# Optimization experiments

Hardware: AMD Instinct MI355X
Metric: run time of the kernel (lower is better)

## Reference

```python
import jax, jax.numpy as jnp
import numpy as np

B, N, D = 8, 4096, 512      # batch, bag_size, model dim (in_dim == att_dim)
H, DH = 8, 64               # heads, dim_head
M = 256                     # landmarks (N % M == 0 -> no padding branch)
PINV_ITERS = 6
CONV_K = 33                 # residual depthwise conv kernel (lucidrains default)


def layernorm(x, g, b, eps=1e-5):
    mu = x.mean(-1, keepdims=True)
    var = ((x - mu) ** 2).mean(-1, keepdims=True)
    return (x - mu) * jax.lax.rsqrt(var + eps) * g + b


def moore_penrose_pinv(x, iters):
    # iterative Newton-Schulz pseudo-inverse, global max normalization as in lucidrains
    abs_x = jnp.abs(x)
    col = abs_x.sum(-1)
    row = abs_x.sum(-2)
    z = jnp.swapaxes(x, -1, -2) / (jnp.max(col) * jnp.max(row))
    I = jnp.eye(x.shape[-1], dtype=x.dtype)
    for _ in range(iters):
        xz = x @ z
        z = 0.25 * z @ (13.0 * I - xz @ (15.0 * I - xz @ (7.0 * I - xz)))
    return z


def setup_inputs() -> dict:
    key = jax.random.key(0)
    ks = jax.random.split(key, 12)
    s = 0.02
    return {
        "X": jax.random.normal(ks[0], (B, N, D), dtype=jnp.float32),
        "Wqkv": jax.random.normal(ks[1], (D, 3 * H * DH), dtype=jnp.float32) * s,
        "Wout": jax.random.normal(ks[2], (H * DH, D), dtype=jnp.float32) * s,
        "bout": jnp.zeros((D,), dtype=jnp.float32),
        "conv_w": jax.random.normal(ks[3], (H, 1, CONV_K, 1), dtype=jnp.float32) * s,
        "g1": jnp.ones((D,), dtype=jnp.float32),
        "beta1": jnp.zeros((D,), dtype=jnp.float32),
        "g2": jnp.ones((D,), dtype=jnp.float32),
        "beta2": jnp.zeros((D,), dtype=jnp.float32),
        "W1": jax.random.normal(ks[4], (D, 4 * D), dtype=jnp.float32) * s,
        "b1": jnp.zeros((4 * D,), dtype=jnp.float32),
        "W2": jax.random.normal(ks[5], (4 * D, D), dtype=jnp.float32) * s,
        "b2": jnp.zeros((D,), dtype=jnp.float32),
    }


def nystrom_attention(x, Wqkv, Wout, bout, conv_w):
    b, n, _ = x.shape
    qkv = x @ Wqkv                                   # (b, n, 3*H*DH)
    qkv = qkv.reshape(b, n, 3, H, DH)
    q = jnp.transpose(qkv[:, :, 0], (0, 2, 1, 3))    # (b, H, n, DH)
    k = jnp.transpose(qkv[:, :, 1], (0, 2, 1, 3))
    v = jnp.transpose(qkv[:, :, 2], (0, 2, 1, 3))
    q = q * (DH ** -0.5)

    l = n // M  # group size per landmark
    q_l = q.reshape(b, H, M, l, DH).mean(axis=3)     # (b, H, M, DH)
    k_l = k.reshape(b, H, M, l, DH).mean(axis=3)

    sim1 = jnp.einsum("bhnd,bhmd->bhnm", q, k_l)     # (b, H, n, M)
    sim2 = jnp.einsum("bhmd,bhld->bhml", q_l, k_l)   # (b, H, M, M)
    sim3 = jnp.einsum("bhmd,bhnd->bhmn", q_l, k)     # (b, H, M, n)

    attn1 = jax.nn.softmax(sim1, axis=-1)
    attn2 = jax.nn.softmax(sim2, axis=-1)
    attn3 = jax.nn.softmax(sim3, axis=-1)

    attn2_inv = moore_penrose_pinv(attn2, PINV_ITERS)
    out = (attn1 @ attn2_inv) @ (attn3 @ v)          # (b, H, n, DH)

    # residual depthwise conv over sequence dim, heads as channels
    res = jax.lax.conv_general_dilated(
        v, conv_w, window_strides=(1, 1),
        padding=((CONV_K // 2, CONV_K // 2), (0, 0)),
        dimension_numbers=("NCHW", "OIHW", "NCHW"),
        feature_group_count=H,
    )
    out = out + res

    out = jnp.transpose(out, (0, 2, 1, 3)).reshape(b, n, H * DH)
    return out @ Wout + bout


def reference(X, Wqkv, Wout, bout, conv_w, g1, beta1, g2, beta2, W1, b1, W2, b2):
    h = layernorm(X, g1, beta1)
    h = nystrom_attention(h, Wqkv, Wout, bout, conv_w)
    # MLP with residual (use_mlp=True); dropout=0.0 -> identity
    m = layernorm(h, g2, beta2)
    m = jax.nn.gelu(m @ W1 + b1, approximate=False) @ W2 + b2
    h = h + m
    # proj_out is Identity since out_dim == att_dim
    return h
```

## Files before the change

### kernel.cpp

```cpp
#include <hip/hip_runtime.h>
#include <hip/hip_bf16.h>
#include <cmath>

#define DEV __device__ __forceinline__

namespace {

constexpr int kB = 8, kN = 4096, kD = 512, kH = 8, kDH = 64, kM = 256, kL = 16, kCK = 33;
constexpr int kBN = kB * kN;
constexpr int kBH = kB * kH;
constexpr int kHD = kH * kDH;
constexpr int kD4 = 4 * kD;
constexpr int kQKVC = 3 * kHD;

typedef __attribute__((ext_vector_type(8))) short short8;
typedef __attribute__((ext_vector_type(4))) float f32x4;

DEV float toF(float x) { return x; }
DEV float toF(__hip_bfloat16 x) { return __bfloat162float(x); }
DEV __hip_bfloat16 f2b(float f) { return __float2bfloat16(f); }
DEV short f2s(float f) {
  __hip_bfloat16 h = __float2bfloat16(f);
  return *reinterpret_cast<short*>(&h);
}
DEV float us2f(unsigned short u) { return __uint_as_float((unsigned)u << 16); }
DEV unsigned short f2us(float f) {
  __hip_bfloat16 h = __float2bfloat16(f);
  return *reinterpret_cast<unsigned short*>(&h);
}

DEV void gload16(const void* g, void* l) {
  __builtin_amdgcn_global_load_lds(
      (const __attribute__((address_space(1))) unsigned*)g,
      (__attribute__((address_space(3))) unsigned*)l, 16, 0, 0);
}

DEV float waveSum(float v) {
#pragma unroll
  for (int o = 32; o > 0; o >>= 1) v += __shfl_down(v, o, 64);
  return v;
}
DEV float waveMax(float v) {
#pragma unroll
  for (int o = 32; o > 0; o >>= 1) v = fmaxf(v, __shfl_down(v, o, 64));
  return v;
}
DEV float blockSum(float v, float* sb) {
  v = waveSum(v);
  int lane = threadIdx.x & 63, w = threadIdx.x >> 6;
  __syncthreads();
  if (lane == 0) sb[w] = v;
  __syncthreads();
  return sb[0] + sb[1] + sb[2] + sb[3];
}
DEV float blockMax(float v, float* sb) {
  v = waveMax(v);
  int lane = threadIdx.x & 63, w = threadIdx.x >> 6;
  __syncthreads();
  if (lane == 0) sb[w] = v;
  __syncthreads();
  return fmaxf(fmaxf(sb[0], sb[1]), fmaxf(sb[2], sb[3]));
}

__global__ __launch_bounds__(256) void detect_k(const unsigned* __restrict__ x,
                                                int* __restrict__ flag) {
  __shared__ int sc[4];
  int t = threadIdx.x;
  int cb = 0;
  for (int i = t; i < 4096; i += 256) {
    unsigned w = x[i];
    float b0 = __uint_as_float(w << 16);
    float b1 = __uint_as_float(w & 0xffff0000u);
    if (fabsf(b0) < 64.0f && (b0 == 0.0f || fabsf(b0) > 1e-20f)) cb++;
    if (fabsf(b1) < 64.0f && (b1 == 0.0f || fabsf(b1) > 1e-20f)) cb++;
  }
#pragma unroll
  for (int o = 32; o > 0; o >>= 1) cb += __shfl_down(cb, o, 64);
  if ((t & 63) == 0) sc[t >> 6] = cb;
  __syncthreads();
  if (t == 0) flag[0] = (sc[0] + sc[1] + sc[2] + sc[3] > 7373) ? 1 : 0;
}

__global__ void cvt_any_k(const void* __restrict__ s, float* __restrict__ d, int n,
                          const int* __restrict__ flag) {
  int i = blockIdx.x * 256 + threadIdx.x;
  if (i >= n) return;
  if (*flag)
    d[i] = toF(((const __hip_bfloat16*)s)[i]);
  else
    d[i] = ((const float*)s)[i];
}

__global__ void cvtT_k(const void* __restrict__ s, __hip_bfloat16* __restrict__ d, int K, int N,
                       const int* __restrict__ flag) {
  int i = blockIdx.x * 256 + threadIdx.x;
  if (i >= N * K) return;
  int n = i / K, k = i - n * K;
  float v = (*flag) ? toF(((const __hip_bfloat16*)s)[(long)k * N + n])
                    : ((const float*)s)[(long)k * N + n];
  d[i] = f2b(v);
}

__global__ void f32tob16_k(const float* __restrict__ s, __hip_bfloat16* __restrict__ d, int n) {
  int i = blockIdx.x * 256 + threadIdx.x;
  if (i < n) d[i] = f2b(s[i]);
}


__global__ __launch_bounds__(256) void ln1_k(const void* __restrict__ xv,
                                             const float* __restrict__ g,
                                             const float* __restrict__ be,
                                             __hip_bfloat16* __restrict__ o,
                                             const int* __restrict__ flag) {
  __shared__ float sb[4];
  size_t row = blockIdx.x;
  __hip_bfloat16* po = o + row * kD;
  int t = threadIdx.x;
  float v0, v1;
  if (*flag) {
    const __hip_bfloat16* pr = (const __hip_bfloat16*)xv + row * kD;
    v0 = toF(pr[t]);
    v1 = toF(pr[t + 256]);
  } else {
    const float* pr = (const float*)xv + row * kD;
    v0 = pr[t];
    v1 = pr[t + 256];
  }
  float s = blockSum(v0 + v1, sb);
  float ss = blockSum(v0 * v0 + v1 * v1, sb);
  float mu = s * (1.0f / kD);
  float var = ss * (1.0f / kD) - mu * mu;
  float rs = rsqrtf(var + 1e-5f);
  po[t] = f2b((v0 - mu) * rs * g[t] + be[t]);
  po[t + 256] = f2b((v1 - mu) * rs * g[t + 256] + be[t + 256]);
}

__global__ __launch_bounds__(256) void ln2_k(const float* __restrict__ x,
                                             const float* __restrict__ g,
                                             const float* __restrict__ be,
                                             __hip_bfloat16* __restrict__ o) {
  __shared__ float sb[4];
  size_t row = blockIdx.x;
  const float* pr = x + row * kD;
  __hip_bfloat16* po = o + row * kD;
  int t = threadIdx.x;
  float v0 = pr[t], v1 = pr[t + 256];
  float s = blockSum(v0 + v1, sb);
  float ss = blockSum(v0 * v0 + v1 * v1, sb);
  float mu = s * (1.0f / kD);
  float var = ss * (1.0f / kD) - mu * mu;
  float rs = rsqrtf(var + 1e-5f);
  po[t] = f2b((v0 - mu) * rs * g[t] + be[t]);
  po[t + 256] = f2b((v1 - mu) * rs * g[t + 256] + be[t + 256]);
}


__global__ void landmark_k(const __hip_bfloat16* __restrict__ src, float* __restrict__ dst) {
  int i = blockIdx.x * 256 + threadIdx.x;
  if (i >= kBH * kM * kDH) return;
  int dh = i & 63, m = (i >> 6) & 255, bh = i >> 14;
  const __hip_bfloat16* p = src + ((size_t)bh * kN + m * kL) * kDH + dh;
  float s = 0.f;
#pragma unroll
  for (int l = 0; l < kL; ++l) s += toF(p[l * kDH]);
  dst[i] = s * (1.0f / kL);
}

__global__ __launch_bounds__(256) void softmax_k(float* __restrict__ X, int ncols) {
  __shared__ float sb[4];
  size_t row = blockIdx.x;
  float* p = X + row * ncols;
  int t = threadIdx.x;
  float mx = -1e30f;
  for (int c = t; c < ncols; c += 256) mx = fmaxf(mx, p[c]);
  mx = blockMax(mx, sb);
  float s = 0.f;
  for (int c = t; c < ncols; c += 256) {
    float e = expf(fminf(p[c] - mx, 0.0f));
    p[c] = e;
    s += e;
  }
  s = blockSum(s, sb);
  float inv = 1.0f / s;
  for (int c = t; c < ncols; c += 256) p[c] *= inv;
}

__global__ __launch_bounds__(256) void pinv_rowcol_k(const float* __restrict__ a2,
                                                     float* __restrict__ rsum,
                                                     float* __restrict__ csum) {
  __shared__ float sb[4];
  int bh = blockIdx.x >> 8, i = blockIdx.x & 255;
  const float* base = a2 + ((size_t)bh << 16);
  int t = threadIdx.x;
  float rs = blockSum(fabsf(base[i * kM + t]), sb);
  float cs = blockSum(fabsf(base[t * kM + i]), sb);
  if (t == 0) {
    rsum[blockIdx.x] = rs;
    csum[blockIdx.x] = cs;
  }
}

__global__ __launch_bounds__(256) void pinv_gmax_k(const float* __restrict__ rsum,
                                                   const float* __restrict__ csum,
                                                   float* __restrict__ gmax) {
  __shared__ float sb[4];
  int t = threadIdx.x;
  float a = 0.f, b = 0.f;
  for (int j = t; j < kBH * kM; j += 256) {
    a = fmaxf(a, rsum[j]);
    b = fmaxf(b, csum[j]);
  }
  a = blockMax(a, sb);
  b = blockMax(b, sb);
  if (t == 0) {
    gmax[0] = a;
    gmax[1] = b;
  }
}

__global__ void pinv_init_k(const float* __restrict__ a2, const float* __restrict__ gmax,
                            __hip_bfloat16* __restrict__ z) {
  int i = blockIdx.x * 256 + threadIdx.x;
  if (i >= kBH * kM * kM) return;
  int col = i & 255, r = (i >> 8) & 255, bh = i >> 16;
  float denom = fmaxf(gmax[0] * gmax[1], 1e-30f);
  z[i] = f2b(a2[((size_t)bh << 16) + col * kM + r] / denom);
}

constexpr int kCR = 128;
constexpr int kCHA = kCK / 2;
constexpr int kCW = kCR + 2 * kCHA;
constexpr int kCP = 72;

__global__ __launch_bounds__(256) void conv_add2_k(const __hip_bfloat16* __restrict__ v,
                                                   const float* __restrict__ w,
                                                   __hip_bfloat16* __restrict__ ao) {
  __shared__ short Vt[kCW * kCP];
  __shared__ float wsh[kCK];
  const int t = threadIdx.x;
  const int bh = blockIdx.x >> 5;
  const int n0 = (blockIdx.x & 31) * kCR;
  const int b = bh >> 3, h = bh & 7;
  if (t < kCK) wsh[t] = w[h * kCK + t];
  const __hip_bfloat16* vbase = v + (size_t)bh * kN * kDH;
#pragma unroll
  for (int u = 0; u < (kCW * 8 + 255) / 256; ++u) {
    const int idx = u * 256 + t;
    if (idx < kCW * 8) {
      const int r = idx >> 3, c8 = (idx & 7) * 8;
      const int n = n0 - kCHA + r;
      uint4 d = {0u, 0u, 0u, 0u};
      if (n >= 0 && n < kN) d = *(const uint4*)(vbase + (size_t)n * kDH + c8);
      *(uint4*)&Vt[r * kCP + c8] = d;
    }
  }
  __syncthreads();
  const int dh8 = (t & 7) * 8;
  const int rg = (t >> 3) * 4;
  float acc[4][8] = {};
#pragma unroll
  for (int wd = 0; wd < kCK + 3; ++wd) {
    short8 v8 = *(const short8*)&Vt[(rg + wd) * kCP + dh8];
    float f[8];
#pragma unroll
    for (int e = 0; e < 8; ++e) f[e] = us2f((unsigned short)v8[e]);
#pragma unroll
    for (int i = 0; i < 4; ++i) {
      const int tap = wd - i;
      if (tap >= 0 && tap < kCK) {
        const float wt = wsh[tap];
#pragma unroll
        for (int e = 0; e < 8; ++e) acc[i][e] = fmaf(f[e], wt, acc[i][e]);
      }
    }
  }
#pragma unroll
  for (int i = 0; i < 4; ++i) {
    const int n = n0 + rg + i;
    __hip_bfloat16* ap = ao + ((size_t)(b * kN + n)) * kHD + h * kDH + dh8;
    uint4 d = *(const uint4*)ap;
    const unsigned short* us = (const unsigned short*)&d;
    unsigned short ov[8];
#pragma unroll
    for (int e = 0; e < 8; ++e) ov[e] = f2us(us2f(us[e]) + acc[i][e]);
    *(uint4*)ap = *(const uint4*)ov;
  }
}

constexpr int FP = 72;

template <bool A3>
__global__ __launch_bounds__(256, 1) void fattn_k(const __hip_bfloat16* __restrict__ Qp,
                                                  const __hip_bfloat16* __restrict__ Kp,
                                                  const __hip_bfloat16* __restrict__ Vp,
                                                  void* __restrict__ Op) {
  __shared__ __align__(16) char smem[111616];
  short* Ks = (short*)smem;
  short* Vs = (short*)(smem + 36864);
  short* Ps = (short*)(smem + 73728);
  float* wred = (float*)(smem + 110592);
  float* Comb = (float*)smem;

  const int t = threadIdx.x;
  const int lane = t & 63, wave = t >> 6;
  const int l15 = lane & 15, quad = lane >> 4;
  const int bh = A3 ? (blockIdx.x >> 2) : (blockIdx.x >> 6);
  const int q0 = A3 ? ((blockIdx.x & 3) * 64) : ((blockIdx.x & 63) * 64);
  const int NTILES = A3 ? (kN / 256) : 1;
  short* Psw = Ps + wave * 64 * FP;

  short8 aq[4][2];
#pragma unroll
  for (int i = 0; i < 4; ++i) {
    const long qrow = (A3 ? ((long)bh * kM) : ((long)bh * kN)) + q0 + i * 16 + l15;
#pragma unroll
    for (int s = 0; s < 2; ++s)
      aq[i][s] = *(const short8*)(Qp + qrow * kDH + quad * 8 + s * 32);
  }

  f32x4 o[4][4] = {};
  float mrow[4][4], lrow[4][4];
#pragma unroll
  for (int i = 0; i < 4; ++i)
#pragma unroll
    for (int rg = 0; rg < 4; ++rg) {
      mrow[i][rg] = -1e30f;
      lrow[i][rg] = 0.f;
    }

  const long kvbase = (long)bh * (A3 ? kN : kM) * kDH;

  for (int tile = 0; tile < NTILES; ++tile) {
    {
      const int r = t >> 2, c = (t & 3) * 16;
#pragma unroll
      for (int p = 0; p < 4; ++p) {
        const int rr = p * 64 + r;
        const long src = kvbase + (long)(tile * 256 + rr) * kDH + c;
        const uint4* ks = (const uint4*)(Kp + src);
        const uint4* vs = (const uint4*)(Vp + src);
        *(uint4*)&Ks[rr * FP + c] = ks[0];
        *(uint4*)&Ks[rr * FP + c + 8] = ks[1];
        *(uint4*)&Vs[rr * FP + c] = vs[0];
        *(uint4*)&Vs[rr * FP + c + 8] = vs[1];
      }
    }
    __syncthreads();

    f32x4 sacc[4][4] = {};
#pragma unroll
    for (int s = 0; s < 2; ++s) {
      short8 bk[4];
#pragma unroll
      for (int j = 0; j < 4; ++j)
        bk[j] = *(const short8*)&Ks[(wave * 64 + j * 16 + l15) * FP + quad * 8 + s * 32];
#pragma unroll
      for (int i = 0; i < 4; ++i)
#pragma unroll
        for (int j = 0; j < 4; ++j)
          sacc[i][j] =
              __builtin_amdgcn_mfma_f32_16x16x32_bf16(aq[i][s], bk[j], sacc[i][j], 0, 0, 0);
    }

    float pmax[4][4];
#pragma unroll
    for (int i = 0; i < 4; ++i)
#pragma unroll
      for (int rg = 0; rg < 4; ++rg) {
        float v = fmaxf(fmaxf(sacc[i][0][rg], sacc[i][1][rg]),
                        fmaxf(sacc[i][2][rg], sacc[i][3][rg]));
#pragma unroll
        for (int d = 1; d < 16; d <<= 1) v = fmaxf(v, __shfl_xor(v, d, 64));
        pmax[i][rg] = v;
      }
    if (l15 == 0) {
#pragma unroll
      for (int i = 0; i < 4; ++i)
#pragma unroll
        for (int rg = 0; rg < 4; ++rg)
          wred[wave * 64 + i * 16 + quad * 4 + rg] = pmax[i][rg];
    }
    __syncthreads();

#pragma unroll
    for (int i = 0; i < 4; ++i)
#pragma unroll
      for (int rg = 0; rg < 4; ++rg) {
        const int row = i * 16 + quad * 4 + rg;
        float tm =
            fmaxf(fmaxf(wred[row], wred[64 + row]), fmaxf(wred[128 + row], wred[192 + row]));
        float mn = fmaxf(mrow[i][rg], tm);
        float c = expf(mrow[i][rg] - mn);
        mrow[i][rg] = mn;
        lrow[i][rg] *= c;
#pragma unroll
        for (int j = 0; j < 4; ++j) o[i][j][rg] *= c;
      }
#pragma unroll
    for (int i = 0; i < 4; ++i)
#pragma unroll
      for (int rg = 0; rg < 4; ++rg) {
        float ls = 0.f;
#pragma unroll
        for (int j = 0; j < 4; ++j) {
          float e = expf(sacc[i][j][rg] - mrow[i][rg]);
          ls += e;
          Psw[(i * 16 + quad * 4 + rg) * FP + j * 16 + l15] = f2s(e);
        }
#pragma unroll
        for (int d = 1; d < 16; d <<= 1) ls += __shfl_xor(ls, d, 64);
        lrow[i][rg] += ls;
      }

#pragma unroll
    for (int s = 0; s < 2; ++s) {
      short8 ap[4];
#pragma unroll
      for (int i = 0; i < 4; ++i)
        ap[i] = *(const short8*)&Psw[(i * 16 + l15) * FP + quad * 8 + s * 32];
      short8 bv[4];
#pragma unroll
      for (int j = 0; j < 4; ++j)
#pragma unroll
        for (int e = 0; e < 8; ++e)
          bv[j][e] = Vs[(wave * 64 + s * 32 + quad * 8 + e) * FP + j * 16 + l15];
#pragma unroll
      for (int i = 0; i < 4; ++i)
#pragma unroll
        for (int j = 0; j < 4; ++j)
          o[i][j] = __builtin_amdgcn_mfma_f32_16x16x32_bf16(ap[i], bv[j], o[i][j], 0, 0, 0);
    }
    __syncthreads();
  }

#pragma unroll
  for (int i = 0; i < 4; ++i)
#pragma unroll
    for (int j = 0; j < 4; ++j)
#pragma unroll
      for (int rg = 0; rg < 4; ++rg)
        Comb[wave * 4096 + (i * 16 + quad * 4 + rg) * 64 + j * 16 + l15] = o[i][j][rg];
  if (l15 == 0) {
#pragma unroll
    for (int i = 0; i < 4; ++i)
#pragma unroll
      for (int rg = 0; rg < 4; ++rg)
        wred[wave * 64 + i * 16 + quad * 4 + rg] = lrow[i][rg];
  }
  __syncthreads();
#pragma unroll
  for (int u = 0; u < 16; ++u) {
    const int idx = u * 256 + t;
    const int row = idx >> 6, dh = idx & 63;
    float v = Comb[idx] + Comb[4096 + idx] + Comb[8192 + idx] + Comb[12288 + idx];
    float linv = 1.0f / (wred[row] + wred[64 + row] + wred[128 + row] + wred[192 + row]);
    if constexpr (A3) {
      ((float*)Op)[((size_t)bh * kM + q0 + row) * kDH + dh] = v * linv;
    } else {
      const int b = bh >> 3, h = bh & 7;
      ((__hip_bfloat16*)Op)[((size_t)(b * kN + q0 + row)) * kHD + h * kDH + dh] =
          f2b(v * linv);
    }
  }
}

constexpr int EPI_F32 = 0, EPI_QKV = 1, EPI_BIAS_F32 = 2, EPI_GELU_BF16 = 3, EPI_RES_OUT = 4,
              EPI_BF16 = 5;

struct EpiArgs {
  const float* bias;
  const float* res;
  __hip_bfloat16* oq;
  __hip_bfloat16* ok;
  __hip_bfloat16* ov;
  __hip_bfloat16* obf;
  void* ovoid;
  const int* flag;
  float eyeC;
  float eyeS;
};

template <int EPI, bool TRB, bool BEYE>
__global__ __launch_bounds__(256) void mgemm_k(const __hip_bfloat16* __restrict__ A, int lda,
                                               long sA, const __hip_bfloat16* __restrict__ B,
                                               int ldb, long sB, float* __restrict__ C, int ldc,
                                               long sC, int K, EpiArgs ep) {
  constexpr int LSA = 32;
  constexpr int LSB = TRB ? 32 : 40;
  __shared__ short As[128 * 32];
  __shared__ short Bs[128 * 40];
  A += (long)blockIdx.z * sA;
  B += (long)blockIdx.z * sB;
  const long cbase = (long)blockIdx.z * sC;
  const int row0 = blockIdx.x * 128, col0 = blockIdx.y * 128;
  const int t = threadIdx.x;
  const int lane = t & 63, wave = t >> 6;
  const int wr = (wave >> 1) * 64, wc = (wave & 1) * 64;
  const int l15 = lane & 15, quad = lane >> 4;
  f32x4 acc[4][4] = {};
  for (int k0 = 0; k0 < K; k0 += 32) {
    {
      const int kc = (t & 3) * 8;
#pragma unroll
      for (int p = 0; p < 2; ++p) {
        const int m = p * 64 + (t >> 2);
        gload16(A + (long)(row0 + m) * lda + k0 + kc, &As[p * 2048 + t * 8]);
      }
    }
    if (TRB) {
      const int kc = (t & 3) * 8;
#pragma unroll
      for (int p = 0; p < 2; ++p) {
        const int n = p * 64 + (t >> 2);
        gload16(B + (long)(col0 + n) * ldb + k0 + kc, &Bs[p * 2048 + t * 8]);
      }
    } else {
      const int k8 = (t & 3) * 8;
#pragma unroll
      for (int p = 0; p < 2; ++p) {
        const int n = p * 64 + (t >> 2);
        short8 vv;
#pragma unroll
        for (int e = 0; e < 8; ++e) {
          float v = toF(B[(long)(k0 + k8 + e) * ldb + col0 + n]);
          if constexpr (BEYE) v = (((k0 + k8 + e) == (col0 + n)) ? ep.eyeC : 0.0f) - v;
          vv[e] = f2s(BEYE ? v * ep.eyeS : v);
        }
        *(short8*)(&Bs[n * LSB + k8]) = vv;
      }
    }
    __syncthreads();
    short8 af[4], bf[4];
#pragma unroll
    for (int i = 0; i < 4; ++i)
      af[i] = *(const short8*)(&As[(wr + i * 16 + l15) * LSA + quad * 8]);
#pragma unroll
    for (int j = 0; j < 4; ++j)
      bf[j] = *(const short8*)(&Bs[(wc + j * 16 + l15) * LSB + quad * 8]);
#pragma unroll
    for (int i = 0; i < 4; ++i)
#pragma unroll
      for (int j = 0; j < 4; ++j)
        acc[i][j] = __builtin_amdgcn_mfma_f32_16x16x32_bf16(af[i], bf[j], acc[i][j], 0, 0, 0);
    __syncthreads();
  }
#pragma unroll
  for (int i = 0; i < 4; ++i) {
#pragma unroll
    for (int j = 0; j < 4; ++j) {
#pragma unroll
      for (int rg = 0; rg < 4; ++rg) {
        int r = row0 + wr + i * 16 + quad * 4 + rg;
        int c = col0 + wc + j * 16 + l15;
        float v = acc[i][j][rg];
        if (EPI == EPI_BF16) {
          ep.obf[cbase + (long)r * ldc + c] = f2b(v);
        } else if (EPI == EPI_QKV) {
          int three = c >> 9, h = (c >> 6) & 7, dh = c & 63;
          int b = r >> 12, n = r & (kN - 1);
          long dst = ((long)(b * kH + h) * kN + n) * kDH + dh;
          if (three == 0)
            ep.oq[dst] = f2b(v * 0.125f);
          else if (three == 1)
            ep.ok[dst] = f2b(v);
          else
            ep.ov[dst] = f2b(v);
        } else if (EPI == EPI_BIAS_F32) {
          C[cbase + (long)r * ldc + c] = v + ep.bias[c];
        } else if (EPI == EPI_GELU_BF16) {
          v += ep.bias[c];
          ep.obf[cbase + (long)r * ldc + c] =
              f2b(0.5f * v * (1.0f + erff(v * 0.70710678118654752f)));
        } else if (EPI == EPI_RES_OUT) {
          long idx = cbase + (long)r * ldc + c;
          float v2 = v + ep.bias[c] + ep.res[idx];
          if (!(v2 == v2)) v2 = 0.0f;
          if (*ep.flag)
            ((__hip_bfloat16*)ep.ovoid)[idx] = f2b(v2);
          else
            ((float*)ep.ovoid)[idx] = v2;
        }
      }
    }
  }
}

template <int EPI, bool TRB, class TAT, class TBT>
__global__ __launch_bounds__(256) void gemm_k(const TAT* __restrict__ A, int lda, long sA,
                                              const TBT* __restrict__ B, int ldb, long sB,
                                              float* __restrict__ C, int ldc, long sC, int K,
                                              EpiArgs ep) {
  __shared__ float As[16][68];
  __shared__ float Bs[16][68];
  A += (long)blockIdx.z * sA;
  B += (long)blockIdx.z * sB;
  const long cbase = (long)blockIdx.z * sC;
  const int row0 = blockIdx.x * 64, col0 = blockIdx.y * 64;
  const int t = threadIdx.x;
  const int ty = t >> 4, tx = t & 15;
  float acc[4][4] = {{0.f, 0.f, 0.f, 0.f}, {0.f, 0.f, 0.f, 0.f},
                     {0.f, 0.f, 0.f, 0.f}, {0.f, 0.f, 0.f, 0.f}};
  const int ka = t & 15, ra = t >> 4;
  for (int k0 = 0; k0 < K; k0 += 16) {
#pragma unroll
    for (int j = 0; j < 4; ++j)
      As[ka][ra + 16 * j] = toF(A[(long)(row0 + ra + 16 * j) * lda + (k0 + ka)]);
    if (TRB) {
#pragma unroll
      for (int j = 0; j < 4; ++j)
        Bs[ka][ra + 16 * j] = toF(B[(long)(col0 + ra + 16 * j) * ldb + (k0 + ka)]);
    } else {
      const int jb = t & 63, kb = t >> 6;
#pragma unroll
      for (int j = 0; j < 4; ++j)
        Bs[kb + 4 * j][jb] = toF(B[(long)(k0 + kb + 4 * j) * ldb + (col0 + jb)]);
    }
    __syncthreads();
#pragma unroll
    for (int kk = 0; kk < 16; ++kk) {
      float av[4], bv[4];
#pragma unroll
      for (int i = 0; i < 4; ++i) av[i] = As[kk][ty * 4 + i];
#pragma unroll
      for (int j = 0; j < 4; ++j) bv[j] = Bs[kk][tx * 4 + j];
#pragma unroll
      for (int i = 0; i < 4; ++i)
#pragma unroll
        for (int j = 0; j < 4; ++j) acc[i][j] += av[i] * bv[j];
    }
    __syncthreads();
  }
#pragma unroll
  for (int i = 0; i < 4; ++i) {
    int r = row0 + ty * 4 + i;
#pragma unroll
    for (int j = 0; j < 4; ++j) {
      int c = col0 + tx * 4 + j;
      C[cbase + (long)r * ldc + c] = acc[i][j];
    }
  }
}

}

extern "C" void kernel_launch(void* const* d_in, const int* in_sizes, int n_in, void* d_out,
                              int out_size, void* d_ws, size_t ws_size, hipStream_t stream) {
  (void)in_sizes; (void)n_in; (void)out_size;

  char* base = (char*)d_ws;
  size_t off = 0;
  auto alloc = [&](size_t bytes) {
    char* p = base + off;
    off = (off + bytes + 255) & ~(size_t)255;
    return p;
  };
  float* a2 = (float*)alloc((size_t)kBH * kM * kM * 4);
  __hip_bfloat16* zs0 = (__hip_bfloat16*)alloc((size_t)kBH * kM * kM * 4);
  __hip_bfloat16* zs1 = (__hip_bfloat16*)alloc((size_t)kBH * kM * kM * 4);
  __hip_bfloat16* zs2 = (__hip_bfloat16*)alloc((size_t)kBH * kM * kM * 4);
  __hip_bfloat16* zs3 = (__hip_bfloat16*)alloc((size_t)kBH * kM * kM * 4);
  __hip_bfloat16* a2b = (__hip_bfloat16*)alloc((size_t)kBH * kM * kM * 2);
  __hip_bfloat16* q = (__hip_bfloat16*)alloc((size_t)kBH * kN * kDH * 2);
  __hip_bfloat16* kk = (__hip_bfloat16*)alloc((size_t)kBH * kN * kDH * 2);
  __hip_bfloat16* vv = (__hip_bfloat16*)alloc((size_t)kBH * kN * kDH * 2);
  __hip_bfloat16* ao = (__hip_bfloat16*)alloc((size_t)kBN * kHD * 2);
  float* ql = (float*)alloc((size_t)kBH * kM * kDH * 4);
  float* kl = (float*)alloc((size_t)kBH * kM * kDH * 4);
  float* w3 = (float*)alloc((size_t)kBH * kM * kDH * 4);
  float* y = (float*)alloc((size_t)kBH * kM * kDH * 4);
  float* rsum = (float*)alloc((size_t)kBH * kM * 4);
  float* csum = (float*)alloc((size_t)kBH * kM * 4);
  float* gmax = (float*)alloc(256);
  int* dflag = (int*)alloc(256);
  __hip_bfloat16* WqkvT = (__hip_bfloat16*)alloc((size_t)kQKVC * kD * 2);
  __hip_bfloat16* WoutT = (__hip_bfloat16*)alloc((size_t)kD * kHD * 2);
  __hip_bfloat16* W1T = (__hip_bfloat16*)alloc((size_t)kD4 * kD * 2);
  __hip_bfloat16* W2T = (__hip_bfloat16*)alloc((size_t)kD * kD4 * 2);
  float* bout_f = (float*)alloc(kD * 4);
  float* b1_f = (float*)alloc(kD4 * 4);
  float* b2_f = (float*)alloc(kD * 4);
  float* convw_f = (float*)alloc(kH * kCK * 4);
  float* g1_f = (float*)alloc(kD * 4);
  float* be1_f = (float*)alloc(kD * 4);
  float* g2_f = (float*)alloc(kD * 4);
  float* be2_f = (float*)alloc(kD * 4);
  __hip_bfloat16* hln = (__hip_bfloat16*)a2;
  float* hbuf = a2;
  __hip_bfloat16* hidden = q;
  __hip_bfloat16* qlb = a2b;
  __hip_bfloat16* klb = a2b + (size_t)kBH * kM * kDH;
  __hip_bfloat16* ylb = a2b + 2 * (size_t)kBH * kM * kDH;
  __hip_bfloat16* hln2 = (__hip_bfloat16*)d_out;

  if (off > ws_size) return;

  detect_k<<<1, 256, 0, stream>>>((const unsigned*)d_in[0], dflag);

  auto cvt = [&](const void* src, float* dst, int n) {
    cvt_any_k<<<(n + 255) / 256, 256, 0, stream>>>(src, dst, n, dflag);
  };
  cvtT_k<<<(kD * kQKVC + 255) / 256, 256, 0, stream>>>(d_in[1], WqkvT, kD, kQKVC, dflag);
  cvtT_k<<<(kHD * kD + 255) / 256, 256, 0, stream>>>(d_in[2], WoutT, kHD, kD, dflag);
  cvtT_k<<<(kD * kD4 + 255) / 256, 256, 0, stream>>>(d_in[9], W1T, kD, kD4, dflag);
  cvtT_k<<<(kD4 * kD + 255) / 256, 256, 0, stream>>>(d_in[11], W2T, kD4, kD, dflag);
  cvt(d_in[3], bout_f, kD);
  cvt(d_in[4], convw_f, kH * kCK);
  cvt(d_in[5], g1_f, kD);
  cvt(d_in[6], be1_f, kD);
  cvt(d_in[7], g2_f, kD);
  cvt(d_in[8], be2_f, kD);
  cvt(d_in[10], b1_f, kD4);
  cvt(d_in[12], b2_f, kD);

  EpiArgs e0 = {};

  ln1_k<<<kBN, 256, 0, stream>>>(d_in[0], g1_f, be1_f, hln, dflag);

  EpiArgs eq = {};
  eq.oq = q; eq.ok = kk; eq.ov = vv;
  mgemm_k<EPI_QKV, true, false>
      <<<dim3(kBN / 128, kQKVC / 128, 1), 256, 0, stream>>>(hln, kD, 0, WqkvT, kD, 0, nullptr, 0,
                                                            0, kD, eq);

  landmark_k<<<(kBH * kM * kDH + 255) / 256, 256, 0, stream>>>(q, ql);
  landmark_k<<<(kBH * kM * kDH + 255) / 256, 256, 0, stream>>>(kk, kl);

  const long sQL = (long)kM * kDH, sA2 = (long)kM * kM;

  gemm_k<EPI_F32, true, float, float><<<dim3(kM / 64, kM / 64, kBH), 256, 0, stream>>>(
      ql, kDH, sQL, kl, kDH, sQL, a2, kM, sA2, kDH, e0);
  softmax_k<<<kBH * kM, 256, 0, stream>>>(a2, kM);

  f32tob16_k<<<(kBH * kM * kM + 255) / 256, 256, 0, stream>>>(a2, a2b, kBH * kM * kM);
  pinv_rowcol_k<<<kBH * kM, 256, 0, stream>>>(a2, rsum, csum);
  pinv_gmax_k<<<1, 256, 0, stream>>>(rsum, csum, gmax);
  pinv_init_k<<<(kBH * kM * kM + 255) / 256, 256, 0, stream>>>(a2, gmax, zs0);

  __hip_bfloat16* bufs[4] = {zs0, zs1, zs2, zs3};
  int zi = 0;
  dim3 gP(kM / 128, kM / 128, kBH);
  for (int it = 0; it < 6; ++it) {
    int o0 = (zi + 1) & 3, o1 = (zi + 2) & 3, o2 = (zi + 3) & 3;
    __hip_bfloat16* Z = bufs[zi];
    __hip_bfloat16* T1 = bufs[o0];
    __hip_bfloat16* T3 = bufs[o1];
    __hip_bfloat16* P3 = bufs[o2];
    EpiArgs ep1 = {}; ep1.obf = T1;
    mgemm_k<EPI_BF16, false, false><<<gP, 256, 0, stream>>>(
        a2b, kM, sA2, Z, kM, sA2, nullptr, kM, sA2, kM, ep1);
    EpiArgs ep2 = {}; ep2.obf = T3; ep2.eyeC = 7.0f; ep2.eyeS = 1.0f;
    mgemm_k<EPI_BF16, false, true><<<gP, 256, 0, stream>>>(
        T1, kM, sA2, T1, kM, sA2, nullptr, kM, sA2, kM, ep2);
    EpiArgs ep3 = {}; ep3.obf = P3; ep3.eyeC = 15.0f; ep3.eyeS = 1.0f;
    mgemm_k<EPI_BF16, false, true><<<gP, 256, 0, stream>>>(
        T1, kM, sA2, T3, kM, sA2, nullptr, kM, sA2, kM, ep3);
    EpiArgs ep4 = {}; ep4.obf = T3; ep4.eyeC = 13.0f; ep4.eyeS = 0.25f;
    mgemm_k<EPI_BF16, false, true><<<gP, 256, 0, stream>>>(
        Z, kM, sA2, P3, kM, sA2, nullptr, kM, sA2, kM, ep4);
    zi = o1;
  }
  __hip_bfloat16* zfin = bufs[zi];

  f32tob16_k<<<(kBH * kM * kDH + 255) / 256, 256, 0, stream>>>(ql, qlb, kBH * kM * kDH);
  f32tob16_k<<<(kBH * kM * kDH + 255) / 256, 256, 0, stream>>>(kl, klb, kBH * kM * kDH);

  fattn_k<true><<<kBH * (kM / 64), 256, 0, stream>>>(qlb, kk, vv, w3);

  gemm_k<EPI_F32, false, __hip_bfloat16, float><<<dim3(kM / 64, 1, kBH), 256, 0, stream>>>(
      zfin, kM, sA2, w3, kDH, sQL, y, kDH, sQL, kM, e0);
  f32tob16_k<<<(kBH * kM * kDH + 255) / 256, 256, 0, stream>>>(y, ylb, kBH * kM * kDH);

  fattn_k<false><<<kBH * (kN / 64), 256, 0, stream>>>(q, klb, ylb, ao);

  conv_add2_k<<<kBH * (kN / kCR), 256, 0, stream>>>(vv, convw_f, ao);

  EpiArgs ew = {}; ew.bias = bout_f;
  mgemm_k<EPI_BIAS_F32, true, false>
      <<<dim3(kBN / 128, kD / 128, 1), 256, 0, stream>>>(ao, kHD, 0, WoutT, kHD, 0, hbuf, kD, 0,
                                                         kHD, ew);

  ln2_k<<<kBN, 256, 0, stream>>>(hbuf, g2_f, be2_f, hln2);
  EpiArgs e1 = {}; e1.bias = b1_f; e1.obf = hidden;
  mgemm_k<EPI_GELU_BF16, true, false>
      <<<dim3(kBN / 128, kD4 / 128, 1), 256, 0, stream>>>(hln2, kD, 0, W1T, kD, 0, nullptr, kD4,
                                                          0, kD, e1);

  EpiArgs e2 = {}; e2.bias = b2_f; e2.res = hbuf; e2.ovoid = d_out; e2.flag = dflag;
  mgemm_k<EPI_RES_OUT, true, false>
      <<<dim3(kBN / 128, kD / 128, 1), 256, 0, stream>>>(hidden, kD4, 0, W2T, kD4, 0, nullptr,
                                                         kD, 0, kD4, e2);
}
```

Before: 1.587 ms.

## Keep transposed copies of pinv iterates so all GEMM operands load row-contiguous

The Newton-Schulz pinv loop previously used a non-transposed B path that gathered eight strided scalar loads per element and applied the eye-minus transform while loading. A new kernel writes each result in both normal and transposed bf16 layouts (the transposed one via an LDS transpose), with the eye/scale transform fused into the transposed store. Every pinv GEMM can then use 16-byte vector loads for both operands. This costs extra writes and LDS per iteration, and the batched/BEYE paths are removed from the general GEMM.

Result: faster. 1.452 ms (-8.5%).

```diff
diff --git a/kernel.cpp b/kernel.cpp
--- a/kernel.cpp
+++ b/kernel.cpp
@@ -218,13 +218,14 @@
   }
 }
 
-__global__ void pinv_init_k(const float* __restrict__ a2, const float* __restrict__ gmax,
-                            __hip_bfloat16* __restrict__ z) {
+__global__ void pinv_init2_k(const float* __restrict__ a2, const float* __restrict__ gmax,
+                             __hip_bfloat16* __restrict__ zn, __hip_bfloat16* __restrict__ zt) {
   int i = blockIdx.x * 256 + threadIdx.x;
   if (i >= kBH * kM * kM) return;
   int col = i & 255, r = (i >> 8) & 255, bh = i >> 16;
-  float denom = fmaxf(gmax[0] * gmax[1], 1e-30f);
-  z[i] = f2b(a2[((size_t)bh << 16) + col * kM + r] / denom);
+  float s = 1.0f / fmaxf(gmax[0] * gmax[1], 1e-30f);
+  zn[i] = f2b(a2[((size_t)bh << 16) + col * kM + r] * s);
+  zt[i] = f2b(a2[i] * s);
 }
 
 constexpr int kCR = 128;
@@ -464,8 +465,8 @@
   }
 }
 
-constexpr int EPI_F32 = 0, EPI_QKV = 1, EPI_BIAS_F32 = 2, EPI_GELU_BF16 = 3, EPI_RES_OUT = 4,
-              EPI_BF16 = 5;
+constexpr int EPI_QKV = 1, EPI_BIAS_F32 = 2, EPI_GELU_BF16 = 3, EPI_RES_OUT = 4;
+constexpr int EPI_F32 = 0;
 
 struct EpiArgs {
   const float* bias;
@@ -476,22 +477,15 @@
   __hip_bfloat16* obf;
   void* ovoid;
   const int* flag;
-  float eyeC;
-  float eyeS;
 };
 
-template <int EPI, bool TRB, bool BEYE>
+template <int EPI>
 __global__ __launch_bounds__(256) void mgemm_k(const __hip_bfloat16* __restrict__ A, int lda,
-                                               long sA, const __hip_bfloat16* __restrict__ B,
-                                               int ldb, long sB, float* __restrict__ C, int ldc,
-                                               long sC, int K, EpiArgs ep) {
-  constexpr int LSA = 32;
-  constexpr int LSB = TRB ? 32 : 40;
+                                               const __hip_bfloat16* __restrict__ B, int ldb,
+                                               float* __restrict__ C, int ldc, int K,
+                                               EpiArgs ep) {
   __shared__ short As[128 * 32];
-  __shared__ short Bs[128 * 40];
-  A += (long)blockIdx.z * sA;
-  B += (long)blockIdx.z * sB;
-  const long cbase = (long)blockIdx.z * sC;
+  __shared__ short Bs[128 * 32];
   const int row0 = blockIdx.x * 128, col0 = blockIdx.y * 128;
   const int t = threadIdx.x;
   const int lane = t & 63, wave = t >> 6;
@@ -499,44 +493,21 @@
   const int l15 = lane & 15, quad = lane >> 4;
   f32x4 acc[4][4] = {};
   for (int k0 = 0; k0 < K; k0 += 32) {
-    {
-      const int kc = (t & 3) * 8;
-#pragma unroll
-      for (int p = 0; p < 2; ++p) {
-        const int m = p * 64 + (t >> 2);
-        gload16(A + (long)(row0 + m) * lda + k0 + kc, &As[p * 2048 + t * 8]);
-      }
-    }
-    if (TRB) {
-      const int kc = (t & 3) * 8;
-#pragma unroll
-      for (int p = 0; p < 2; ++p) {
-        const int n = p * 64 + (t >> 2);
-        gload16(B + (long)(col0 + n) * ldb + k0 + kc, &Bs[p * 2048 + t * 8]);
-      }
-    } else {
-      const int k8 = (t & 3) * 8;
-#pragma unroll
-      for (int p = 0; p < 2; ++p) {
-        const int n = p * 64 + (t >> 2);
-        short8 vv;
-#pragma unroll
-        for (int e = 0; e < 8; ++e) {
-          float v = toF(B[(long)(k0 + k8 + e) * ldb + col0 + n]);
-          if constexpr (BEYE) v = (((k0 + k8 + e) == (col0 + n)) ? ep.eyeC : 0.0f) - v;
-          vv[e] = f2s(BEYE ? v * ep.eyeS : v);
-        }
-        *(short8*)(&Bs[n * LSB + k8]) = vv;
-      }
+    const int kc = (t & 3) * 8;
+#pragma unroll
+    for (int p = 0; p < 2; ++p) {
+      const int m = p * 64 + (t >> 2);
+      gload16(A + (long)(row0 + m) * lda + k0 + kc, &As[p * 2048 + t * 8]);
+      gload16(B + (long)(col0 + m) * ldb + k0 + kc, &Bs[p * 2048 + t * 8]);
     }
     __syncthreads();
     short8 af[4], bf[4];
 #pragma unroll
     for (int i = 0; i < 4; ++i)
-      af[i] = *(const short8*)(&As[(wr + i * 16 + l15) * LSA + quad * 8]);
+      af[i] = *(const short8*)(&As[(wr + i * 16 + l15) * 32 + quad * 8]);
 #pragma unroll
     for (int j = 0; j < 4; ++j)
-      bf[j] = *(const short8*)(&Bs[(wc + j * 16 + l15) * LSB + quad * 8]);
+      bf[j] = *(const short8*)(&Bs[(wc + j * 16 + l15) * 32 + quad * 8]);
 #pragma unroll
     for (int i = 0; i < 4; ++i)
 #pragma unroll
@@ -553,9 +524,7 @@
         int r = row0 + wr + i * 16 + quad * 4 + rg;
         int c = col0 + wc + j * 16 + l15;
         float v = acc[i][j][rg];
-        if (EPI == EPI_BF16) {
-          ep.obf[cbase + (long)r * ldc + c] = f2b(v);
-        } else if (EPI == EPI_QKV) {
+        if (EPI == EPI_QKV) {
           int three = c >> 9, h = (c >> 6) & 7, dh = c & 63;
           int b = r >> 12, n = r & (kN - 1);
           long dst = ((long)(b * kH + h) * kN + n) * kDH + dh;
@@ -566,13 +535,13 @@
           else
             ep.ov[dst] = f2b(v);
         } else if (EPI == EPI_BIAS_F32) {
-          C[cbase + (long)r * ldc + c] = v + ep.bias[c];
+          C[(long)r * ldc + c] = v + ep.bias[c];
         } else if (EPI == EPI_GELU_BF16) {
           v += ep.bias[c];
-          ep.obf[cbase + (long)r * ldc + c] =
+          ep.obf[(long)r * ldc + c] =
               f2b(0.5f * v * (1.0f + erff(v * 0.70710678118654752f)));
         } else if (EPI == EPI_RES_OUT) {
-          long idx = cbase + (long)r * ldc + c;
+          long idx = (long)r * ldc + c;
           float v2 = v + ep.bias[c] + ep.res[idx];
           if (!(v2 == v2)) v2 = 0.0f;
           if (*ep.flag)
@@ -582,6 +551,83 @@
         }
       }
     }
+  }
+}
+
+template <bool WN>
+__global__ __launch_bounds__(256) void mgemmT_k(const __hip_bfloat16* __restrict__ A,
+                                                const __hip_bfloat16* __restrict__ B,
+                                                __hip_bfloat16* __restrict__ Cn,
+                                                __hip_bfloat16* __restrict__ Ct,
+                                                float eyeC, float eyeS, float oscl) {
+  constexpr int TS = 136;
+  __shared__ short sm[128 * TS];
+  short* As = sm;
+  short* Bs = sm + 4096;
+  const long mbase = (long)blockIdx.z * ((long)kM * kM);
+  const int row0 = blockIdx.x * 128, col0 = blockIdx.y * 128;
+  const int t = threadIdx.x;
+  const int lane = t & 63, wave = t >> 6;
+  const int wr = (wave >> 1) * 64, wc = (wave & 1) * 64;
+  const int l15 = lane & 15, quad = lane >> 4;
+  f32x4 acc[4][4] = {};
+  for (int k0 = 0; k0 < kM; k0 += 32) {
+    const int kc = (t & 3) * 8;
+#pragma unroll
+    for (int p = 0; p < 2; ++p) {
+      const int m = p * 64 + (t >> 2);
+      gload16(A + mbase + (long)(row0 + m) * kM + k0 + kc, &As[p * 2048 + t * 8]);
+      gload16(B + mbase + (long)(col0 + m) * kM + k0 + kc, &Bs[p * 2048 + t * 8]);
+    }
+    __syncthreads();
+    short8 af[4], bf[4];
+#pragma unroll
+    for (int i = 0; i < 4; ++i)
+      af[i] = *(const short8*)(&As[(wr + i * 16 + l15) * 32 + quad * 8]);
+#pragma unroll
+    for (int j = 0; j < 4; ++j)
+      bf[j] = *(const short8*)(&Bs[(wc + j * 16 + l15) * 32 + quad * 8]);
+#pragma unroll
+    for (int i = 0; i < 4; ++i)
+#pragma unroll
+      for (int j = 0; j < 4; ++j)
+        acc[i][j] = __builtin_amdgcn_mfma_f32_16x16x32_bf16(af[i], bf[j], acc[i][j], 0, 0, 0);
+    __syncthreads();
+  }
+  if (WN) {
+#pragma unroll
+    for (int i = 0; i < 4; ++i)
+#pragma unroll
+      for (int j = 0; j < 4; ++j)
+#pragma unroll
+        for (int rg = 0; rg < 4; ++rg) {
+          int r = row0 + wr + i * 16 + quad * 4 + rg;
+          int c = col0 + wc + j * 16 + l15;
+          Cn[mbase + (long)r * kM + c] = f2b(acc[i][j][rg] * oscl);
+        }
+  }
+#pragma unroll
+  for (int i = 0; i < 4; ++i)
+#pragma unroll
+    for (int j = 0; j < 4; ++j) {
+      const int rl0 = wr + i * 16 + quad * 4;
+      const int cl = wc + j * 16 + l15;
+      const int r0 = row0 + rl0, c = col0 + cl;
+      short pk[4];
+#pragma unroll
+      for (int rg = 0; rg < 4; ++rg) {
+        float v = (((r0 + rg) == c) ? eyeC : 0.0f) - acc[i][j][rg];
+        pk[rg] = f2s(v * eyeS);
+      }
+      *(ulong1*)&sm[cl * TS + rl0] = *(const ulong1*)pk;
+    }
+  __syncthreads();
+#pragma unroll
+  for (int u = 0; u < 8; ++u) {
+    const int rowt = u * 16 + (t >> 4);
+    const int c8 = (t & 15) * 8;
+    uint4 d = *(const uint4*)&sm[rowt * TS + c8];
+    *(uint4*)(Ct + mbase + (long)(col0 + rowt) * kM + row0 + c8) = d;
   }
 }
 
@@ -654,12 +700,10 @@
     off = (off + bytes + 255) & ~(size_t)255;
     return p;
   };
-  float* a2 = (float*)alloc((size_t)kBH * kM * kM * 4);
-  __hip_bfloat16* zs0 = (__hip_bfloat16*)alloc((size_t)kBH * kM * kM * 4);
-  __hip_bfloat16* zs1 = (__hip_bfloat16*)alloc((size_t)kBH * kM * kM * 4);
-  __hip_bfloat16* zs2 = (__hip_bfloat16*)alloc((size_t)kBH * kM * kM * 4);
-  __hip_bfloat16* zs3 = (__hip_bfloat16*)alloc((size_t)kBH * kM * kM * 4);
-  __hip_bfloat16* a2b = (__hip_bfloat16*)alloc((size_t)kBH * kM * kM * 2);
+  const size_t kMat = (size_t)kBH * kM * kM;
+  float* a2 = (float*)alloc(kMat * 4);
+  __hip_bfloat16* mb0 = (__hip_bfloat16*)alloc(kMat * 2 * 8);
+  __hip_bfloat16* a2b = (__hip_bfloat16*)alloc(kMat * 2);
   __hip_bfloat16* q = (__hip_bfloat16*)alloc((size_t)kBH * kN * kDH * 2);
   __hip_bfloat16* kk = (__hip_bfloat16*)alloc((size_t)kBH * kN * kDH * 2);
   __hip_bfloat16* vv = (__hip_bfloat16*)alloc((size_t)kBH * kN * kDH * 2);
@@ -684,6 +728,7 @@
   float* be1_f = (float*)alloc(kD * 4);
   float* g2_f = (float*)alloc(kD * 4);
   float* be2_f = (float*)alloc(kD * 4);
+  auto mb = [&](int i) { return mb0 + (size_t)i * kMat; };
   __hip_bfloat16* hln = (__hip_bfloat16*)a2;
   float* hbuf = a2;
   __hip_bfloat16* hidden = q;
@@ -718,9 +763,8 @@
 
   EpiArgs eq = {};
   eq.oq = q; eq.ok = kk; eq.ov = vv;
-  mgemm_k<EPI_QKV, true, false>
-      <<<dim3(kBN / 128, kQKVC / 128, 1), 256, 0, stream>>>(hln, kD, 0, WqkvT, kD, 0, nullptr, 0,
-                                                            0, kD, eq);
+  mgemm_k<EPI_QKV><<<dim3(kBN / 128, kQKVC / 128, 1), 256, 0, stream>>>(hln, kD, WqkvT, kD,
+                                                                        nullptr, 0, kD, eq);
 
   landmark_k<<<(kBH * kM * kDH + 255) / 256, 256, 0, stream>>>(q, ql);
   landmark_k<<<(kBH * kM * kDH + 255) / 256, 256, 0, stream>>>(kk, kl);
@@ -731,35 +775,26 @@
       ql, kDH, sQL, kl, kDH, sQL, a2, kM, sA2, kDH, e0);
   softmax_k<<<kBH * kM, 256, 0, stream>>>(a2, kM);
 
-  f32tob16_k<<<(kBH * kM * kM + 255) / 256, 256, 0, stream>>>(a2, a2b, kBH * kM * kM);
+  f32tob16_k<<<((int)kMat + 255) / 256, 256, 0, stream>>>(a2, a2b, (int)kMat);
   pinv_rowcol_k<<<kBH * kM, 256, 0, stream>>>(a2, rsum, csum);
   pinv_gmax_k<<<1, 256, 0, stream>>>(rsum, csum, gmax);
-  pinv_init_k<<<(kBH * kM * kM + 255) / 256, 256, 0, stream>>>(a2, gmax, zs0);
-
-  __hip_bfloat16* bufs[4] = {zs0, zs1, zs2, zs3};
-  int zi = 0;
-  dim3 gP(kM / 128, kM / 128, kBH);
-  for (int it = 0; it < 6; ++it) {
-    int o0 = (zi + 1) & 3, o1 = (zi + 2) & 3, o2 = (zi + 3) & 3;
-    __hip_bfloat16* Z = bufs[zi];
-    __hip_bfloat16* T1 = bufs[o0];
-    __hip_bfloat16* T3 = bufs[o1];
-    __hip_bfloat16* P3 = bufs[o2];
-    EpiArgs ep1 = {}; ep1.obf = T1;
-    mgemm_k<EPI_BF16, false, false><<<gP, 256, 0, stream>>>(
-        a2b, kM, sA2, Z, kM, sA2, nullptr, kM, sA2, kM, ep1);
-    EpiArgs ep2 = {}; ep2.obf = T3; ep2.eyeC = 7.0f; ep2.eyeS = 1.0f;
-    mgemm_k<EPI_BF16, false, true><<<gP, 256, 0, stream>>>(
-        T1, kM, sA2, T1, kM, sA2, nullptr, kM, sA2, kM, ep2);
-    EpiArgs ep3 = {}; ep3.obf = P3; ep3.eyeC = 15.0f; ep3.eyeS = 1.0f;
-    mgemm_k<EPI_BF16, false, true><<<gP, 256, 0, stream>>>(
-        T1, kM, sA2, T3, kM, sA2, nullptr, kM, sA2, kM, ep3);
-    EpiArgs ep4 = {}; ep4.obf = T3; ep4.eyeC = 13.0f; ep4.eyeS = 0.25f;
-    mgemm_k<EPI_BF16, false, true><<<gP, 256, 0, stream>>>(
-        Z, kM, sA2, P3, kM, sA2, nullptr, kM, sA2, kM, ep4);
-    zi = o1;
-  }
-  __hip_bfloat16* zfin = bufs[zi];
+  pinv_init2_k<<<((int)kMat + 255) / 256, 256, 0, stream>>>(a2, gmax, mb(0), mb(1));
+
+  {
+    __hip_bfloat16 *Zc = mb(0), *ZcT = mb(1), *Zn = mb(6), *ZnT = mb(7);
+    __hip_bfloat16 *T1 = mb(2), *T1E = mb(3), *T3E = mb(4), *P3E = mb(5);
+    dim3 gP(kM / 128, kM / 128, kBH);
+    for (int it = 0; it < 6; ++it) {
+      mgemmT_k<true><<<gP, 256, 0, stream>>>(a2b, ZcT, T1, T1E, 7.0f, 1.0f, 1.0f);
+      mgemmT_k<false><<<gP, 256, 0, stream>>>(T1, T1E, nullptr, T3E, 15.0f, 1.0f, 1.0f);
+      mgemmT_k<false><<<gP, 256, 0, stream>>>(T1, T3E, nullptr, P3E, 13.0f, 1.0f, 1.0f);
+      mgemmT_k<true><<<gP, 256, 0, stream>>>(Zc, P3E, Zn, ZnT, 0.0f, -0.25f, 0.25f);
+      __hip_bfloat16* tp;
+      tp = Zc; Zc = Zn; Zn = tp;
+      tp = ZcT; ZcT = ZnT; ZnT = tp;
+    }
+  }
+  __hip_bfloat16* zfin = mb(0);
 
   f32tob16_k<<<(kBH * kM * kDH + 255) / 256, 256, 0, stream>>>(ql, qlb, kBH * kM * kDH);
   f32tob16_k<<<(kBH * kM * kDH + 255) / 256, 256, 0, stream>>>(kl, klb, kBH * kM * kDH);
@@ -775,18 +810,15 @@
   conv_add2_k<<<kBH * (kN / kCR), 256, 0, stream>>>(vv, convw_f, ao);
 
   EpiArgs ew = {}; ew.bias = bout_f;
-  mgemm_k<EPI_BIAS_F32, true, false>
-      <<<dim3(kBN / 128, kD / 128, 1), 256, 0, stream>>>(ao, kHD, 0, WoutT, kHD, 0, hbuf, kD, 0,
-                                                         kHD, ew);
+  mgemm_k<EPI_BIAS_F32><<<dim3(kBN / 128, kD / 128, 1), 256, 0, stream>>>(ao, kHD, WoutT, kHD,
+                                                                          hbuf, kD, kHD, ew);
 
   ln2_k<<<kBN, 256, 0, stream>>>(hbuf, g2_f, be2_f, hln2);
   EpiArgs e1 = {}; e1.bias = b1_f; e1.obf = hidden;
-  mgemm_k<EPI_GELU_BF16, true, false>
-      <<<dim3(kBN / 128, kD4 / 128, 1), 256, 0, stream>>>(hln2, kD, 0, W1T, kD, 0, nullptr, kD4,
-                                                          0, kD, e1);
+  mgemm_k<EPI_GELU_BF16><<<dim3(kBN / 128, kD4 / 128, 1), 256, 0, stream>>>(
+      hln2, kD, W1T, kD, nullptr, kD4, kD, e1);
 
   EpiArgs e2 = {}; e2.bias = b2_f; e2.res = hbuf; e2.ovoid = d_out; e2.flag = dflag;
-  mgemm_k<EPI_RES_OUT, true, false>
-      <<<dim3(kBN / 128, kD / 128, 1), 256, 0, stream>>>(hidden, kD4, 0, W2T, kD4, 0, nullptr,
-                                                         kD, 0, kD4, e2);
-}
+  mgemm_k<EPI_RES_OUT><<<dim3(kBN / 128, kD / 128, 1), 256, 0, stream>>>(
+      hidden, kD4, W2T, kD4, nullptr, kD, kD4, e2);
+}
```
